# Performance work log

Hardware: AMD Instinct MI355X
Metric: run time of the kernel (lower is better)

## Reference

```python
import jax, jax.numpy as jnp
import numpy as np

N, D_IN, D_OUT, A, B = 100000, 128, 64, 8, 512
F = 2 * D_OUT  # feature_dim = output_dim * 2


def setup_inputs() -> dict:
    key = jax.random.key(0)
    ks = jax.random.split(key, 6)
    x = jax.random.normal(ks[0], (N, D_IN), jnp.float32)
    batch = jnp.sort(jax.random.randint(ks[1], (N,), 0, B)).astype(jnp.int32)
    def lin(k, out_d, in_d):
        return jax.random.normal(k, (out_d, in_d), jnp.float32) / np.float32(np.sqrt(in_d))
    W_in = lin(ks[2], F, D_IN)
    b_in = jnp.zeros((F,), jnp.float32)
    W_a = lin(ks[3], A, F)
    b_a = jnp.zeros((A,), jnp.float32)
    h_dim = 2 * F * A + D_IN + F
    W_out = lin(ks[4], D_OUT, h_dim)
    b_out = jnp.zeros((D_OUT,), jnp.float32)
    return {"x": x, "batch": batch, "num_segments": B,
            "W_in": W_in, "b_in": b_in, "W_a": W_a, "b_a": b_a,
            "W_out": W_out, "b_out": b_out}


def reference(x, batch, num_segments, W_in, b_in, W_a, b_a, W_out, b_out):
    # transform_in
    xp = x @ W_in.T + b_in                          # [N, F]
    # aggregator_activation('potential') = exp(-|.|)
    score = jnp.exp(-jnp.abs(xp @ W_a.T + b_a))     # [N, A]
    # einsum('nf,na->afn') materialized as [N, A, F] (node-major for segment ops)
    e = score[:, :, None] * xp[:, None, :]          # [N, A, F]
    seg_sum = jax.ops.segment_sum(e, batch, num_segments=num_segments)      # [B, A, F]
    counts = jax.ops.segment_sum(jnp.ones((e.shape[0], 1, 1), e.dtype), batch,
                                 num_segments=num_segments)                  # [B, 1, 1]
    mean_p = seg_sum / jnp.maximum(counts, 1.0)
    max_p = jax.ops.segment_max(e, batch, num_segments=num_segments)        # [B, A, F]
    max_p = jnp.where(counts > 0, max_p, 0.0)
    # cat along feature dim then flatten (A, 2F) -> matches torch transpose+cat+reshape
    agg = jnp.concatenate([mean_p, max_p], axis=-1).reshape(num_segments, -1)  # [B, 2*F*A]
    H = jnp.concatenate([x, xp, agg[batch]], axis=-1)  # [N, D_IN + F + 2*F*A]
    return jax.nn.relu(H @ W_out.T + b_out)            # [N, D_OUT]
```

## Files before the change

kernel.cpp:

```cpp
#include <hip/hip_runtime.h>
#include <math.h>

#define N_NODES 100000
#define D_INPUT 128
#define FDIM 128
#define A_HEADS 8
#define B_SEGS 512
#define D_OUTPUT 64
#define H_DIM 2304

typedef __attribute__((ext_vector_type(8))) __bf16 bf16x8;
typedef __attribute__((ext_vector_type(4))) float f32x4;

static __device__ inline unsigned short f2bfu(float f) {
    unsigned u = __builtin_bit_cast(unsigned, f);
    u += 0x7fffu + ((u >> 16) & 1u);
    return (unsigned short)(u >> 16);
}
static __device__ inline unsigned packbf(float a, float b) {
    return (unsigned)f2bfu(a) | ((unsigned)f2bfu(b) << 16);
}
static __device__ inline float bfl(unsigned u) {
    unsigned x = u << 16; return __builtin_bit_cast(float, x);
}
static __device__ inline float bfh(unsigned u) {
    unsigned x = u & 0xffff0000u; return __builtin_bit_cast(float, x);
}
static __device__ inline bf16x8 pack8(float4 a, float4 b) {
    union { unsigned u[4]; bf16x8 v; } r;
    r.u[0] = packbf(a.x, a.y); r.u[1] = packbf(a.z, a.w);
    r.u[2] = packbf(b.x, b.y); r.u[3] = packbf(b.z, b.w);
    return r.v;
}

__global__ void seg_bounds_kernel(const int* __restrict__ batch, int n,
                                  int* __restrict__ seg_start) {
    int b = threadIdx.x;
    if (b > B_SEGS) return;
    int lo = 0, hi = n;
    while (lo < hi) {
        int mid = (lo + hi) >> 1;
        if (batch[mid] < b) lo = mid + 1; else hi = mid;
    }
    seg_start[b] = lo;
}

__global__ __launch_bounds__(256) void wconv_kernel(
        const float* __restrict__ W_in, const float* __restrict__ W_a,
        const float* __restrict__ W_out, unsigned* __restrict__ Wb,
        unsigned* __restrict__ Wa, unsigned* __restrict__ Wo,
        unsigned* __restrict__ Wagg) {
    int i = blockIdx.x * 256 + threadIdx.x;
    if (i < 8192) {
        float2 v = *(const float2*)(W_in + (size_t)i * 2);
        Wb[i] = packbf(v.x, v.y);
    } else if (i < 9216) {
        int j = i - 8192;
        if (j < 512) {
            float2 v = *(const float2*)(W_a + (size_t)j * 2);
            Wa[j] = packbf(v.x, v.y);
        } else Wa[j] = 0u;
    } else if (i < 17408) {
        int j = i - 9216;
        int row = j >> 7, cu = j & 127;
        float2 v = *(const float2*)(W_out + (size_t)row * H_DIM + cu * 2);
        Wo[j] = packbf(v.x, v.y);
    } else if (i < 82944) {
        int j = i - 17408;
        int row = j >> 10, cu = j & 1023;
        float2 v = *(const float2*)(W_out + (size_t)row * H_DIM + 256 + cu * 2);
        Wagg[j] = packbf(v.x, v.y);
    }
}

__global__ __launch_bounds__(1024) void mega_kernel(
        const float* __restrict__ x, const int* __restrict__ seg_start,
        const float* __restrict__ b_in, const float* __restrict__ b_a,
        const float* __restrict__ b_out, const unsigned* __restrict__ Wb,
        const unsigned* __restrict__ Wa, const unsigned* __restrict__ Wo,
        const unsigned* __restrict__ Wagg, unsigned* __restrict__ out_part_u32,
        float* __restrict__ out) {
    __shared__ __align__(16) unsigned WbL[128 * 68];
    __shared__ __align__(16) unsigned WaL[16 * 68];
    __shared__ __align__(16) unsigned WoL[64 * 132];
    __shared__ __align__(16) unsigned XP[256 * 68];
    __shared__ float scoref[256 * 8];
    __shared__ float projL[64];
    unsigned short* XPs = (unsigned short*)XP;
    float* XPf = (float*)XP;
    unsigned short* opart16 = (unsigned short*)out_part_u32;

    const int b = blockIdx.x;
    const int s0 = seg_start[b], s1 = seg_start[b + 1];
    const int cnt = s1 - s0;
    if (cnt == 0) return;
    const int t = threadIdx.x;
    const int last_c0 = s0 + ((cnt - 1) >> 8) * 256;

    const int w = t >> 6, l = t & 63, lr = l & 15, lk = l >> 4;
    const int q4 = l & 15, gq = l >> 4, a0h = w & 7, gh = w >> 3;
    const int g = gh * 4 + gq;

    {
        const uint4* srcb = (const uint4*)Wb;
#pragma unroll
        for (int i = 0; i < 2; ++i) {
            int idx = i * 1024 + t;
            int row = idx >> 4, c4 = idx & 15;
            *(uint4*)&WbL[row * 68 + c4 * 4] = srcb[idx];
        }
        const uint4* srco = (const uint4*)Wo;
#pragma unroll
        for (int i = 0; i < 2; ++i) {
            int idx = i * 1024 + t;
            int row = idx >> 5, c4 = idx & 31;
            *(uint4*)&WoL[row * 132 + c4 * 4] = srco[idx];
        }
        if (t < 256) {
            const uint4* sa = (const uint4*)Wa;
            int row = t >> 4, c4 = t & 15;
            *(uint4*)&WaL[row * 68 + c4 * 4] = sa[t];
        }
    }
    bf16x8 af[4];
    {
        const int arowc = min(s0 + w * 16 + lr, s1 - 1);
#pragma unroll
        for (int ks = 0; ks < 4; ++ks) {
            const float4* xp4 = (const float4*)(x + (size_t)arowc * 128 + ks * 32 + lk * 8);
            af[ks] = pack8(xp4[0], xp4[1]);
        }
    }
    __syncthreads();

    float binv[8];
#pragma unroll
    for (int nr = 0; nr < 8; ++nr) binv[nr] = b_in[nr * 16 + lr];
    const float ba = b_a[lr & 7];

    const f32x4 z4 = {0.f, 0.f, 0.f, 0.f};
    float sm[8], mx[8];
#pragma unroll
    for (int j = 0; j < 8; ++j) { sm[j] = 0.f; mx[j] = -INFINITY; }
    f32x4 aco[4];

    for (int c0 = s0; c0 < s1; c0 += 256) {
        const int rc = min(256, s1 - c0);
        if (c0 != s0) {
            const int arowc = min(c0 + w * 16 + lr, s1 - 1);
#pragma unroll
            for (int ks = 0; ks < 4; ++ks) {
                const float4* xp4 = (const float4*)(x + (size_t)arowc * 128 + ks * 32 + lk * 8);
                af[ks] = pack8(xp4[0], xp4[1]);
            }
        }

#pragma unroll
        for (int nh = 0; nh < 2; ++nh) {
            f32x4 acc[4];
#pragma unroll
            for (int nr = 0; nr < 4; ++nr) acc[nr] = z4;
#pragma unroll
            for (int ks = 0; ks < 4; ++ks)
#pragma unroll
                for (int nr = 0; nr < 4; ++nr) {
                    bf16x8 bfrag = *(const bf16x8*)&WbL[((nh * 4 + nr) * 16 + lr) * 68 + ks * 16 + lk * 4];
                    acc[nr] = __builtin_amdgcn_mfma_f32_16x16x32_bf16(af[ks], bfrag, acc[nr], 0, 0, 0);
                }
#pragma unroll
            for (int nr = 0; nr < 4; ++nr)
#pragma unroll
                for (int r = 0; r < 4; ++r) {
                    int row = w * 16 + lk * 4 + r;
                    XPs[row * 136 + (nh * 4 + nr) * 16 + lr] =
                        f2bfu(((const float*)&acc[nr])[r] + binv[nh * 4 + nr]);
                }
        }
        bf16x8 xf[4];
#pragma unroll
        for (int ks = 0; ks < 4; ++ks)
            xf[ks] = *(const bf16x8*)&XPs[(w * 16 + lr) * 136 + ks * 32 + lk * 8];
        f32x4 sacc = z4;
#pragma unroll
        for (int ks = 0; ks < 4; ++ks) {
            bf16x8 bfrag = *(const bf16x8*)&WaL[lr * 68 + ks * 16 + lk * 4];
            sacc = __builtin_amdgcn_mfma_f32_16x16x32_bf16(xf[ks], bfrag, sacc, 0, 0, 0);
        }
        if (lr < A_HEADS) {
#pragma unroll
            for (int r = 0; r < 4; ++r) {
                int row = w * 16 + lk * 4 + r;
                scoref[row * 8 + lr] = __expf(-fabsf(((const float*)&sacc)[r] + ba));
            }
        }
#pragma unroll
        for (int nr = 0; nr < 4; ++nr) aco[nr] = z4;
#pragma unroll
        for (int ks = 0; ks < 4; ++ks)
#pragma unroll
            for (int nr = 0; nr < 4; ++nr) {
                bf16x8 b0 = *(const bf16x8*)&WoL[(nr * 16 + lr) * 132 + ks * 16 + lk * 4];
                aco[nr] = __builtin_amdgcn_mfma_f32_16x16x32_bf16(af[ks], b0, aco[nr], 0, 0, 0);
                bf16x8 b1 = *(const bf16x8*)&WoL[(nr * 16 + lr) * 132 + 64 + ks * 16 + lk * 4];
                aco[nr] = __builtin_amdgcn_mfma_f32_16x16x32_bf16(xf[ks], b1, aco[nr], 0, 0, 0);
            }
        if (c0 != last_c0) {
#pragma unroll
            for (int nr = 0; nr < 4; ++nr)
#pragma unroll
                for (int r = 0; r < 4; ++r) {
                    int n = c0 + w * 16 + lk * 4 + r;
                    opart16[(size_t)n * 64 + nr * 16 + lr] = f2bfu(((const float*)&aco[nr])[r]);
                }
        }
        __syncthreads();

        for (int i = g; i < rc; i += 8) {
            uint4 v = *(const uint4*)&XP[i * 68 + q4 * 4];
            float sa = scoref[i * 8 + a0h];
            float e;
            e = sa * bfl(v.x); sm[0] += e; mx[0] = fmaxf(mx[0], e);
            e = sa * bfh(v.x); sm[1] += e; mx[1] = fmaxf(mx[1], e);
            e = sa * bfl(v.y); sm[2] += e; mx[2] = fmaxf(mx[2], e);
            e = sa * bfh(v.y); sm[3] += e; mx[3] = fmaxf(mx[3], e);
            e = sa * bfl(v.z); sm[4] += e; mx[4] = fmaxf(mx[4], e);
            e = sa * bfh(v.z); sm[5] += e; mx[5] = fmaxf(mx[5], e);
            e = sa * bfl(v.w); sm[6] += e; mx[6] = fmaxf(mx[6], e);
            e = sa * bfh(v.w); sm[7] += e; mx[7] = fmaxf(mx[7], e);
        }
        if (c0 + 256 < s1) __syncthreads();
    }

#pragma unroll
    for (int d = 16; d <= 32; d <<= 1)
#pragma unroll
        for (int j = 0; j < 8; ++j) {
            sm[j] += __shfl_xor(sm[j], d);
            mx[j] = fmaxf(mx[j], __shfl_xor(mx[j], d));
        }
    __syncthreads();
    if (gh == 1 && l < 16) {
        float* dst = &scoref[(a0h * 16 + l) * 16];
        *(float4*)&dst[0]  = make_float4(sm[0], sm[1], sm[2], sm[3]);
        *(float4*)&dst[4]  = make_float4(sm[4], sm[5], sm[6], sm[7]);
        *(float4*)&dst[8]  = make_float4(mx[0], mx[1], mx[2], mx[3]);
        *(float4*)&dst[12] = make_float4(mx[4], mx[5], mx[6], mx[7]);
    }
    __syncthreads();
    if (gh == 0 && l < 16) {
        const float* src = &scoref[(a0h * 16 + l) * 16];
        float4 s0v = *(const float4*)&src[0], s1v = *(const float4*)&src[4];
        float4 m0v = *(const float4*)&src[8], m1v = *(const float4*)&src[12];
        const float inv = 1.f / (float)cnt;
        float4 a0o = make_float4((sm[0] + s0v.x) * inv, (sm[1] + s0v.y) * inv,
                                 (sm[2] + s0v.z) * inv, (sm[3] + s0v.w) * inv);
        float4 a1o = make_float4((sm[4] + s1v.x) * inv, (sm[5] + s1v.y) * inv,
                                 (sm[6] + s1v.z) * inv, (sm[7] + s1v.w) * inv);
        *(float4*)&XPf[a0h * 256 + l * 8]     = a0o;
        *(float4*)&XPf[a0h * 256 + l * 8 + 4] = a1o;
        *(float4*)&XPf[a0h * 256 + 128 + l * 8] =
            make_float4(fmaxf(mx[0], m0v.x), fmaxf(mx[1], m0v.y),
                        fmaxf(mx[2], m0v.z), fmaxf(mx[3], m0v.w));
        *(float4*)&XPf[a0h * 256 + 128 + l * 8 + 4] =
            make_float4(fmaxf(mx[4], m1v.x), fmaxf(mx[5], m1v.y),
                        fmaxf(mx[6], m1v.z), fmaxf(mx[7], m1v.w));
    }
    __syncthreads();

#pragma unroll
    for (int i = 0; i < 4; ++i) {
        int o = w * 4 + i;
        const unsigned* wrow = Wagg + (size_t)o * 1024;
        float partial = 0.f;
#pragma unroll
        for (int c = 0; c < 4; ++c) {
            int j4 = c * 256 + l * 4;
            uint4 wv = *(const uint4*)&wrow[j4];
            const float* av = &XPf[2 * j4];
            partial = fmaf(bfl(wv.x), av[0], partial);
            partial = fmaf(bfh(wv.x), av[1], partial);
            partial = fmaf(bfl(wv.y), av[2], partial);
            partial = fmaf(bfh(wv.y), av[3], partial);
            partial = fmaf(bfl(wv.z), av[4], partial);
            partial = fmaf(bfh(wv.z), av[5], partial);
            partial = fmaf(bfl(wv.w), av[6], partial);
            partial = fmaf(bfh(wv.w), av[7], partial);
        }
#pragma unroll
        for (int m = 1; m < 64; m <<= 1) partial += __shfl_xor(partial, m);
        if (l == 0) projL[o] = partial + b_out[o];
    }
    __syncthreads();

    {
        const int rr = t >> 3, cg = t & 7;
        float p[8];
#pragma unroll
        for (int j = 0; j < 8; ++j) p[j] = projL[cg * 8 + j];
        for (int row = s0 + rr; row < last_c0; row += 128) {
            uint4 v = *(const uint4*)&out_part_u32[(size_t)row * 32 + cg * 4];
            float4 o0, o1;
            o0.x = fmaxf(bfl(v.x) + p[0], 0.f);
            o0.y = fmaxf(bfh(v.x) + p[1], 0.f);
            o0.z = fmaxf(bfl(v.y) + p[2], 0.f);
            o0.w = fmaxf(bfh(v.y) + p[3], 0.f);
            o1.x = fmaxf(bfl(v.z) + p[4], 0.f);
            o1.y = fmaxf(bfh(v.z) + p[5], 0.f);
            o1.z = fmaxf(bfl(v.w) + p[6], 0.f);
            o1.w = fmaxf(bfh(v.w) + p[7], 0.f);
            *(float4*)&out[(size_t)row * 64 + cg * 8] = o0;
            *(float4*)&out[(size_t)row * 64 + cg * 8 + 4] = o1;
        }
    }
    {
        float pj[4];
#pragma unroll
        for (int nr = 0; nr < 4; ++nr) pj[nr] = projL[nr * 16 + lr];
#pragma unroll
        for (int r = 0; r < 4; ++r) {
            int n = last_c0 + w * 16 + lk * 4 + r;
            if (n < s1) {
#pragma unroll
                for (int nr = 0; nr < 4; ++nr)
                    out[(size_t)n * 64 + nr * 16 + lr] =
                        fmaxf(((const float*)&aco[nr])[r] + pj[nr], 0.f);
            }
        }
    }
}

extern "C" void kernel_launch(void* const* d_in, const int* in_sizes, int n_in,
                              void* d_out, int out_size, void* d_ws, size_t ws_size,
                              hipStream_t stream) {
    const float* x     = (const float*)d_in[0];
    const int*   batch = (const int*)d_in[1];
    const float* W_in  = (const float*)d_in[3];
    const float* b_in  = (const float*)d_in[4];
    const float* W_a   = (const float*)d_in[5];
    const float* b_a   = (const float*)d_in[6];
    const float* W_out = (const float*)d_in[7];
    const float* b_out = (const float*)d_in[8];
    float* out = (float*)d_out;

    int* seg_start  = (int*)d_ws;
    unsigned* Wb    = (unsigned*)(seg_start + 520);
    unsigned* Wa    = Wb + 8192;
    unsigned* Wo    = Wa + 1024;
    unsigned* Wagg  = Wo + 8192;
    unsigned* out_part_u32 = Wagg + 65536;

    seg_bounds_kernel<<<1, 1024, 0, stream>>>(batch, N_NODES, seg_start);
    wconv_kernel<<<324, 256, 0, stream>>>(W_in, W_a, W_out, Wb, Wa, Wo, Wagg);
    mega_kernel<<<B_SEGS, 1024, 0, stream>>>(
        x, seg_start, b_in, b_a, b_out, Wb, Wa, Wo, Wagg, out_part_u32, out);
}
```

Before: 61.57 us.

## Swizzle XP shared layout, fold segment bounds into weight conversion kernel

Drops the padded row stride of the XP shared tile and uses an XOR swizzle on 16-byte chunks instead. This reduces LDS footprint and is meant to avoid bank conflicts on the MFMA stores and the aggregation reads. The score buffer stride becomes 9 to spread banks. The separate segment-bounds launch is merged into an extra block of the weight-conversion kernel, saving one launch. The float-to-bf16 conversion now uses the compiler's native cast instead of manual rounding.

Result: slower. 67.11 us (+9.0%).

```diff
diff --git a/kernel.cpp b/kernel.cpp
--- a/kernel.cpp
+++ b/kernel.cpp
@@ -13,9 +13,7 @@
 typedef __attribute__((ext_vector_type(4))) float f32x4;
 
 static __device__ inline unsigned short f2bfu(float f) {
-    unsigned u = __builtin_bit_cast(unsigned, f);
-    u += 0x7fffu + ((u >> 16) & 1u);
-    return (unsigned short)(u >> 16);
+    return __builtin_bit_cast(unsigned short, (__bf16)f);
 }
 static __device__ inline unsigned packbf(float a, float b) {
     return (unsigned)f2bfu(a) | ((unsigned)f2bfu(b) << 16);
@@ -33,23 +31,23 @@
     return r.v;
 }
 
-__global__ void seg_bounds_kernel(const int* __restrict__ batch, int n,
-                                  int* __restrict__ seg_start) {
-    int b = threadIdx.x;
-    if (b > B_SEGS) return;
-    int lo = 0, hi = n;
-    while (lo < hi) {
-        int mid = (lo + hi) >> 1;
-        if (batch[mid] < b) lo = mid + 1; else hi = mid;
-    }
-    seg_start[b] = lo;
-}
-
 __global__ __launch_bounds__(256) void wconv_kernel(
         const float* __restrict__ W_in, const float* __restrict__ W_a,
-        const float* __restrict__ W_out, unsigned* __restrict__ Wb,
-        unsigned* __restrict__ Wa, unsigned* __restrict__ Wo,
-        unsigned* __restrict__ Wagg) {
+        const float* __restrict__ W_out, const int* __restrict__ batch,
+        unsigned* __restrict__ Wb, unsigned* __restrict__ Wa,
+        unsigned* __restrict__ Wo, unsigned* __restrict__ Wagg,
+        int* __restrict__ seg_start) {
+    if (blockIdx.x == 324) {
+        for (int b = threadIdx.x; b <= B_SEGS; b += 256) {
+            int lo = 0, hi = N_NODES;
+            while (lo < hi) {
+                int mid = (lo + hi) >> 1;
+                if (batch[mid] < b) lo = mid + 1; else hi = mid;
+            }
+            seg_start[b] = lo;
+        }
+        return;
+    }
     int i = blockIdx.x * 256 + threadIdx.x;
     if (i < 8192) {
         float2 v = *(const float2*)(W_in + (size_t)i * 2);
@@ -83,8 +81,8 @@
     __shared__ __align__(16) unsigned WbL[128 * 68];
     __shared__ __align__(16) unsigned WaL[16 * 68];
     __shared__ __align__(16) unsigned WoL[64 * 132];
-    __shared__ __align__(16) unsigned XP[256 * 68];
-    __shared__ float scoref[256 * 8];
+    __shared__ __align__(16) unsigned XP[256 * 64];
+    __shared__ float scoref[256 * 9];
     __shared__ float projL[64];
     unsigned short* XPs = (unsigned short*)XP;
     float* XPf = (float*)XP;
@@ -168,18 +166,24 @@
                     acc[nr] = __builtin_amdgcn_mfma_f32_16x16x32_bf16(af[ks], bfrag, acc[nr], 0, 0, 0);
                 }
 #pragma unroll
-            for (int nr = 0; nr < 4; ++nr)
+            for (int nr = 0; nr < 4; ++nr) {
+                const int col = (nh * 4 + nr) * 16 + lr;
+                const int col8 = col >> 3, c7 = col & 7;
 #pragma unroll
                 for (int r = 0; r < 4; ++r) {
                     int row = w * 16 + lk * 4 + r;
-                    XPs[row * 136 + (nh * 4 + nr) * 16 + lr] =
+                    XPs[row * 128 + ((col8 ^ (row & 7)) << 3) + c7] =
                         f2bfu(((const float*)&acc[nr])[r] + binv[nh * 4 + nr]);
                 }
+            }
         }
         bf16x8 xf[4];
-#pragma unroll
-        for (int ks = 0; ks < 4; ++ks)
-            xf[ks] = *(const bf16x8*)&XPs[(w * 16 + lr) * 136 + ks * 32 + lk * 8];
+        {
+            const int xrow = w * 16 + lr, rs = lr & 7;
+#pragma unroll
+            for (int ks = 0; ks < 4; ++ks)
+                xf[ks] = *(const bf16x8*)&XPs[xrow * 128 + (((ks * 4 + lk) ^ rs) << 3)];
+        }
         f32x4 sacc = z4;
 #pragma unroll
         for (int ks = 0; ks < 4; ++ks) {
@@ -190,7 +194,7 @@
 #pragma unroll
             for (int r = 0; r < 4; ++r) {
                 int row = w * 16 + lk * 4 + r;
-                scoref[row * 8 + lr] = __expf(-fabsf(((const float*)&sacc)[r] + ba));
+                scoref[row * 9 + lr] = __expf(-fabsf(((const float*)&sacc)[r] + ba));
             }
         }
 #pragma unroll
@@ -216,8 +220,8 @@
         __syncthreads();
 
         for (int i = g; i < rc; i += 8) {
-            uint4 v = *(const uint4*)&XP[i * 68 + q4 * 4];
-            float sa = scoref[i * 8 + a0h];
+            uint4 v = *(const uint4*)&XP[i * 64 + ((q4 ^ (i & 7)) << 2)];
+            float sa = scoref[i * 9 + a0h];
             float e;
             e = sa * bfl(v.x); sm[0] += e; mx[0] = fmaxf(mx[0], e);
             e = sa * bfh(v.x); sm[1] += e; mx[1] = fmaxf(mx[1], e);
@@ -349,8 +353,8 @@
     unsigned* Wagg  = Wo + 8192;
     unsigned* out_part_u32 = Wagg + 65536;
 
-    seg_bounds_kernel<<<1, 1024, 0, stream>>>(batch, N_NODES, seg_start);
-    wconv_kernel<<<324, 256, 0, stream>>>(W_in, W_a, W_out, Wb, Wa, Wo, Wagg);
+    wconv_kernel<<<325, 256, 0, stream>>>(W_in, W_a, W_out, batch,
+                                          Wb, Wa, Wo, Wagg, seg_start);
     mega_kernel<<<B_SEGS, 1024, 0, stream>>>(
         x, seg_start, b_in, b_a, b_out, Wb, Wa, Wo, Wagg, out_part_u32, out);
 }
```
